# Kernel optimization log

Measured on AMD Instinct MI355X. Metric: run time of the kernel, lower is better.

Reference implementation:

```python
import jax, jax.numpy as jnp
import numpy as np

# pywt Wavelet('db4') decomposition filters (8 taps)
DEC_LO = jnp.array([-0.010597401784997278, 0.032883011666982945, 0.030841381835986965,
                    -0.18703481171888114, -0.02798376941698385, 0.6308807679295904,
                    0.7148465705525415, 0.23037781330885523], dtype=jnp.float32)
DEC_HI = jnp.array([-0.23037781330885523, 0.7148465705525415, -0.6308807679295904,
                    -0.02798376941698385, 0.18703481171888114, 0.030841381835986965,
                    -0.032883011666982945, -0.010597401784997278], dtype=jnp.float32)
FLEN = 8
LEVEL = 3


def _dwt_last(x, f):
    """Single-level DWT along last axis, pywt 'symmetric' mode.
    out[i] = sum_k f[k] * ext[2i+1-k] (true convolution, downsample by 2)."""
    p = FLEN - 1
    pad = [(0, 0)] * (x.ndim - 1) + [(p, p)]
    xp = jnp.pad(x, pad, mode='symmetric')[..., 1:]
    n = x.shape[-1]
    out_len = (n + FLEN - 1) // 2
    f_rev = f[::-1]
    y = f_rev[0] * xp[..., 0:2 * out_len:2]
    for j in range(1, FLEN):  # fixed 8-tap loop
        y = y + f_rev[j] * xp[..., j:j + 2 * out_len:2]
    return y


def _dwt_h(x, f):
    # DWT along axis -2 (rows/H)
    return jnp.swapaxes(_dwt_last(jnp.swapaxes(x, -1, -2), f), -1, -2)


def _dwt2(x):
    # x: [B, H, W] -> (cA, cH, cV, cD), matching pywt dwt2 ('aa','da','ad','dd')
    lo_w = _dwt_last(x, DEC_LO)
    hi_w = _dwt_last(x, DEC_HI)
    cA = _dwt_h(lo_w, DEC_LO)  # low H,  low W
    cH = _dwt_h(lo_w, DEC_HI)  # high H, low W  (horizontal detail)
    cV = _dwt_h(hi_w, DEC_LO)  # low H,  high W (vertical detail)
    cD = _dwt_h(hi_w, DEC_HI)  # high H, high W (diagonal detail)
    return cA, cH, cV, cD


def setup_inputs() -> dict:
    key = jax.random.key(0)
    x = jax.random.normal(key, (16, 1, 1024, 1024), dtype=jnp.float32)
    return {"x": x}


def reference(x):
    # wavedec2 ordering: (cA_L, (cH_L, cV_L, cD_L), ..., (cH_1, cV_1, cD_1))
    a = x[:, 0]  # [B, H, W]
    details = []
    for _ in range(LEVEL):
        a, lh, hl, hh = _dwt2(a)
        details.insert(0, (lh, hl, hh))  # coarsest first, as pywt returns
    outs = [a[:, None]]  # [B,1,h,w]
    for lh, hl, hh in details:
        outs += [lh[:, None], hl[:, None], hh[:, None]]
    return tuple(outs)
```

## Files before the change

### kernel.cpp

```cpp
#include <hip/hip_runtime.h>

typedef float f4 __attribute__((ext_vector_type(4)));
typedef f4 f4u __attribute__((aligned(4)));

__device__ __forceinline__ int refl(int i, int n) {
    i = (i < 0) ? (-i - 1) : i;
    i = (i >= n) ? (2 * n - 1 - i) : i;
    return i;
}

__device__ __forceinline__ unsigned bpack(float lo, float hi) {
    union { float f; unsigned u; } a, b;
    a.f = lo; b.f = hi;
    const unsigned ua = (a.u + 0x7FFFu + ((a.u >> 16) & 1u)) >> 16;
    const unsigned ub = (b.u + 0x7FFFu + ((b.u >> 16) & 1u)) & 0xFFFF0000u;
    return ua | ub;
}
__device__ __forceinline__ float b_lo(unsigned u) {
    union { unsigned u; float f; } x; x.u = u << 16; return x.f;
}
__device__ __forceinline__ float b_hi(unsigned u) {
    union { unsigned u; float f; } x; x.u = u & 0xFFFF0000u; return x.f;
}

__device__ __constant__ const float LOF[8] = {
    -0.010597401784997278f,  0.032883011666982945f,
     0.030841381835986965f, -0.18703481171888114f,
    -0.02798376941698385f,   0.6308807679295904f,
     0.7148465705525415f,    0.23037781330885523f };
__device__ __constant__ const float HIF[8] = {
    -0.23037781330885523f,   0.7148465705525415f,
    -0.6308807679295904f,   -0.02798376941698385f,
     0.18703481171888114f,   0.030841381835986965f,
    -0.032883011666982945f, -0.010597401784997278f };

template<int N, int LDIN, int M, int RPB>
__global__ __launch_bounds__(256, 3)
void dwt_stripe(const float* __restrict__ in, int inb,
                float* __restrict__ oA, int ldA, int Ab,
                float* __restrict__ oH, float* __restrict__ oV,
                float* __restrict__ oD)
{
    constexpr int NG  = (M + 7) / 8;
    constexpr int LDP = 8 * NG;
    constexpr int S   = (M + RPB - 1) / RPB;
    constexpr int HR  = 2 * RPB + 6;
    constexpr int GHI = (N - 16) / 16;
    constexpr int NGI = GHI;
    static_assert(NG - 1 == GHI + 1, "expect exactly 2 edge groups");
    constexpr int NAI = HR * NGI;
    constexpr int NAT = NAI + HR * 2;
    constexpr int NQF = M / 4;
    constexpr int TC  = M - 4 * NQF;
    constexpr int NBM = (RPB / 2) * NQF;
    constexpr int NBT2 = (RPB / 2) * TC;
    constexpr int NB  = NBM + NBT2;

    __shared__ unsigned s[HR * LDP];

    const int G = gridDim.x;
    const int q = G >> 3, rm = G & 7;
    const int xcd = blockIdx.x & 7, pos = blockIdx.x >> 3;
    const int sid = xcd * q + (xcd < rm ? xcd : rm) + pos;
    const int sy = sid % S, b = sid / S;

    const int tid = threadIdx.x;
    const int gr0 = RPB * sy;
    const int rb  = 2 * gr0 - 6;
    const float* Ain = in + b * inb;

    #pragma unroll
    for (int k = 0; k < (NAT + 255) / 256; ++k) {
        const int item = k * 256 + tid;
        if (item < NAI) {
            const int tr = item / NGI;
            const int g  = 1 + (item - tr * NGI);
            const int rr = refl(rb + tr, N);
            const float* p = Ain + rr * LDIN + (16 * g - 8);
            float v[24];
            #pragma unroll
            for (int j = 0; j < 6; ++j) {
                const float4 t4 = *(const float4*)(p + 4 * j);
                v[4*j] = t4.x; v[4*j+1] = t4.y; v[4*j+2] = t4.z; v[4*j+3] = t4.w;
            }
            unsigned w[8];
            #pragma unroll
            for (int d = 0; d < 8; ++d) {
                float lo = 0.f, hi = 0.f;
                #pragma unroll
                for (int t = 0; t < 8; ++t) {
                    const float x = v[2 * d + 9 - t];
                    lo += LOF[t] * x;
                    hi += HIF[t] * x;
                }
                w[d] = bpack(lo, hi);
            }
            unsigned* dst = &s[tr * LDP + 8 * g];
            *(uint4*)(dst)     = make_uint4(w[0], w[1], w[2], w[3]);
            *(uint4*)(dst + 4) = make_uint4(w[4], w[5], w[6], w[7]);
        } else if (item < NAT) {
            const int e  = item - NAI;
            const int tr = e >> 1;
            const int g  = (e & 1) ? (GHI + 1) : 0;
            const int rr = refl(rb + tr, N);
            const float* row = Ain + rr * LDIN;
            const int cb = 16 * g - 8;
            float v[24];
            #pragma unroll
            for (int u = 0; u < 24; ++u) v[u] = row[refl(cb + u, N)];
            unsigned w[8];
            #pragma unroll
            for (int d = 0; d < 8; ++d) {
                float lo = 0.f, hi = 0.f;
                #pragma unroll
                for (int t = 0; t < 8; ++t) {
                    const float x = v[2 * d + 9 - t];
                    lo += LOF[t] * x;
                    hi += HIF[t] * x;
                }
                w[d] = bpack(lo, hi);
            }
            unsigned* dst = &s[tr * LDP + 8 * g];
            *(uint4*)(dst)     = make_uint4(w[0], w[1], w[2], w[3]);
            *(uint4*)(dst + 4) = make_uint4(w[4], w[5], w[6], w[7]);
        }
    }
    __syncthreads();

    #pragma unroll
    for (int k = 0; k < (NB + 255) / 256; ++k) {
        const int item = k * 256 + tid;
        if (item < NBM) {
            const int pr = item / NQF, qc = item - pr * NQF;
            uint4 qv[10];
            #pragma unroll
            for (int j = 0; j < 10; ++j)
                qv[j] = *(const uint4*)&s[(4 * pr + j) * LDP + 4 * qc];

            #pragma unroll
            for (int d = 0; d < 2; ++d) {
                const int gr = gr0 + 2 * pr + d;
                if (gr >= M) continue;
                f4 vA = 0.f, vH = 0.f, vV = 0.f, vD = 0.f;
                #pragma unroll
                for (int t = 0; t < 8; ++t) {
                    const uint4 qq = qv[2 * d + 7 - t];
                    f4 lo, hi;
                    lo.x = b_lo(qq.x); lo.y = b_lo(qq.y); lo.z = b_lo(qq.z); lo.w = b_lo(qq.w);
                    hi.x = b_hi(qq.x); hi.y = b_hi(qq.y); hi.z = b_hi(qq.z); hi.w = b_hi(qq.w);
                    vA += LOF[t] * lo;  vH += HIF[t] * lo;
                    vV += LOF[t] * hi;  vD += HIF[t] * hi;
                }
                const int cq = 4 * qc;
                *(f4u*)&oA[b * Ab + gr * ldA + cq] = vA;
                const int od = b * (M * M) + gr * M + cq;
                *(f4u*)&oH[od] = vH;
                *(f4u*)&oV[od] = vV;
                *(f4u*)&oD[od] = vD;
            }
        } else if (item < NB) {
            const int e = item - NBM;
            const int pr = e % (RPB / 2), c = 4 * NQF + e / (RPB / 2);
            float lov[10], hiv[10];
            #pragma unroll
            for (int j = 0; j < 10; ++j) {
                const unsigned u = s[(4 * pr + j) * LDP + c];
                lov[j] = b_lo(u); hiv[j] = b_hi(u);
            }
            float A0=0.f,H0=0.f,V0=0.f,D0=0.f,A1=0.f,H1=0.f,V1=0.f,D1=0.f;
            #pragma unroll
            for (int t = 0; t < 8; ++t) {
                const float l0 = lov[7 - t], h0 = hiv[7 - t];
                const float l1 = lov[9 - t], h1 = hiv[9 - t];
                A0 += LOF[t] * l0;  H0 += HIF[t] * l0;
                V0 += LOF[t] * h0;  D0 += HIF[t] * h0;
                A1 += LOF[t] * l1;  H1 += HIF[t] * l1;
                V1 += LOF[t] * h1;  D1 += HIF[t] * h1;
            }
            const int gr = gr0 + 2 * pr;
            const int od = b * (M * M) + gr * M + c;
            if (gr < M) {
                oA[b * Ab + gr * ldA + c] = A0;
                oH[od] = H0; oV[od] = V0; oD[od] = D0;
            }
            if (gr + 1 < M) {
                oA[b * Ab + (gr + 1) * ldA + c] = A1;
                oH[od + M] = H1; oV[od + M] = V1; oD[od + M] = D1;
            }
        }
    }
}

#define NTF 512
__global__ __launch_bounds__(NTF, 8)
void dwt2_fused(const float* __restrict__ in, int n, int ldin, int inb,
                int m, int nty, int ntx,
                float* __restrict__ oA, int ldA, int Ab,
                float* __restrict__ oH, float* __restrict__ oV,
                float* __restrict__ oD)
{
    __shared__ unsigned s[70 * 36];

    const int G = gridDim.x;
    const int q = G >> 3, rm = G & 7;
    const int xcd = blockIdx.x & 7, pos = blockIdx.x >> 3;
    const int i = xcd * q + (xcd < rm ? xcd : rm) + pos;
    const int ty = i % nty;
    const int t2 = i / nty;
    const int tx = t2 % ntx;
    const int b  = t2 / ntx;

    const int tid = threadIdx.x;
    const int c0 = tx * 32, r0 = ty * 32;
    const float* Ain = in + b * inb;

    const int rb  = 2 * r0 - 6;
    const int cw0 = 2 * c0 - 8;
    const bool interior = (rb >= 0) && (rb + 69 < n) && (cw0 >= 0) && (cw0 + 71 < n);

    const int tr0 = tid >> 3, g0 = tid & 7;
    const bool has2 = (tid < 48);
    const int tr1 = 64 + (tid >> 3), g1 = tid & 7;

    float v0[16], v1[16];
    if (interior) {
        const float* p0 = Ain + (rb + tr0) * ldin + (cw0 + 8 * g0);
        const float4 a0 = ((const float4*)p0)[0];
        const float4 a1 = ((const float4*)p0)[1];
        const float4 a2 = ((const float4*)p0)[2];
        const float4 a3 = ((const float4*)p0)[3];
        v0[0]=a0.x; v0[1]=a0.y; v0[2]=a0.z; v0[3]=a0.w;
        v0[4]=a1.x; v0[5]=a1.y; v0[6]=a1.z; v0[7]=a1.w;
        v0[8]=a2.x; v0[9]=a2.y; v0[10]=a2.z; v0[11]=a2.w;
        v0[12]=a3.x; v0[13]=a3.y; v0[14]=a3.z; v0[15]=a3.w;
        if (has2) {
            const float* p1 = Ain + (rb + tr1) * ldin + (cw0 + 8 * g1);
            const float4 b0 = ((const float4*)p1)[0];
            const float4 b1 = ((const float4*)p1)[1];
            const float4 b2 = ((const float4*)p1)[2];
            const float4 b3 = ((const float4*)p1)[3];
            v1[0]=b0.x; v1[1]=b0.y; v1[2]=b0.z; v1[3]=b0.w;
            v1[4]=b1.x; v1[5]=b1.y; v1[6]=b1.z; v1[7]=b1.w;
            v1[8]=b2.x; v1[9]=b2.y; v1[10]=b2.z; v1[11]=b2.w;
            v1[12]=b3.x; v1[13]=b3.y; v1[14]=b3.z; v1[15]=b3.w;
        }
    } else {
        const float* row0 = Ain + refl(rb + tr0, n) * ldin;
        const int cb0 = cw0 + 8 * g0;
        #pragma unroll
        for (int u = 0; u < 16; ++u) v0[u] = row0[refl(cb0 + u, n)];
        if (has2) {
            const float* row1 = Ain + refl(rb + tr1, n) * ldin;
            const int cb1 = cw0 + 8 * g1;
            #pragma unroll
            for (int u = 0; u < 16; ++u) v1[u] = row1[refl(cb1 + u, n)];
        }
    }

    {
        unsigned w[4];
        #pragma unroll
        for (int d = 0; d < 4; ++d) {
            float lo = 0.f, hi = 0.f;
            #pragma unroll
            for (int t = 0; t < 8; ++t) {
                const float x = v0[2 * d + 9 - t];
                lo += LOF[t] * x;
                hi += HIF[t] * x;
            }
            w[d] = bpack(lo, hi);
        }
        *(uint4*)&s[tr0 * 36 + 4 * g0] = make_uint4(w[0], w[1], w[2], w[3]);
    }
    if (has2) {
        unsigned w[4];
        #pragma unroll
        for (int d = 0; d < 4; ++d) {
            float lo = 0.f, hi = 0.f;
            #pragma unroll
            for (int t = 0; t < 8; ++t) {
                const float x = v1[2 * d + 9 - t];
                lo += LOF[t] * x;
                hi += HIF[t] * x;
            }
            w[d] = bpack(lo, hi);
        }
        *(uint4*)&s[tr1 * 36 + 4 * g1] = make_uint4(w[0], w[1], w[2], w[3]);
    }
    __syncthreads();

    const int c = tid & 31, pr = tid >> 5;
    float lov[10], hiv[10];
    #pragma unroll
    for (int j = 0; j < 10; ++j) {
        const unsigned u = s[(4 * pr + j) * 36 + c];
        lov[j] = b_lo(u); hiv[j] = b_hi(u);
    }
    float A0=0.f,H0=0.f,V0=0.f,D0=0.f,A1=0.f,H1=0.f,V1=0.f,D1=0.f;
    #pragma unroll
    for (int t = 0; t < 8; ++t) {
        const float l0 = lov[7 - t], h0 = hiv[7 - t];
        const float l1 = lov[9 - t], h1 = hiv[9 - t];
        A0 += LOF[t] * l0;  H0 += HIF[t] * l0;
        V0 += LOF[t] * h0;  D0 += HIF[t] * h0;
        A1 += LOF[t] * l1;  H1 += HIF[t] * l1;
        V1 += LOF[t] * h1;  D1 += HIF[t] * h1;
    }
    const int gr = r0 + 2 * pr, gc = c0 + c;
    if (gc < m) {
        const int ob = b * (m * m);
        const int od = ob + gr * m + gc;
        if (gr < m) {
            oA[b * Ab + gr * ldA + gc] = A0;
            oH[od] = H0; oV[od] = V0; oD[od] = D0;
        }
        if (gr + 1 < m) {
            oA[b * Ab + (gr + 1) * ldA + gc] = A1;
            oH[od + m] = H1; oV[od + m] = V1; oD[od + m] = D1;
        }
    }
}

extern "C" void kernel_launch(void* const* d_in, const int* in_sizes, int n_in,
                              void* d_out, int out_size, void* d_ws, size_t ws_size,
                              hipStream_t stream) {
    const float* x = (const float*)d_in[0];
    float* out = (float*)d_out;
    float* ws  = (float*)d_ws;

    const int B = 16;
    const int m1 = 515, m2 = 261, m3 = 134;
    const int n2 = 515, n3 = 261;

    const int ld1 = 516, b1 = m1 * ld1;
    const int ld2 = 264, b2 = m2 * ld2;
    float* a1 = ws;
    float* a2 = ws + (size_t)b1 * B;

    const size_t sz1 = (size_t)B * m1 * m1;
    const size_t sz2 = (size_t)B * m2 * m2;
    const size_t sz3 = (size_t)B * m3 * m3;

    float* a3  = out;
    float* lh3 = a3  + sz3;
    float* hl3 = lh3 + sz3;
    float* hh3 = hl3 + sz3;
    float* lh2 = hh3 + sz3;
    float* hl2 = lh2 + sz2;
    float* hh2 = hl2 + sz2;
    float* lh1 = hh2 + sz2;
    float* hl1 = lh1 + sz1;
    float* hh1 = hl1 + sz1;

    const int S1 = (m1 + 7) / 8;
    const int t2_ = (m2 + 31) / 32;
    const int t3  = (m3 + 31) / 32;

    dim3 blk(256);
    dwt_stripe<1024, 1024, 515, 8><<<dim3(S1 * B), blk, 0, stream>>>(
        x, 1024 * 1024, a1, ld1, b1, lh1, hl1, hh1);

    dwt2_fused<<<dim3(t2_ * t2_ * B), dim3(NTF), 0, stream>>>(
        a1, n2, ld1, b1, m2, t2_, t2_,
        a2, ld2, b2, lh2, hl2, hh2);

    dwt2_fused<<<dim3(t3 * t3 * B), dim3(NTF), 0, stream>>>(
        a2, n3, ld2, b2, m3, t3, t3,
        a3, m3, m3 * m3, lh3, hl3, hh3);
}
```

Baseline: 52.39 us.

## Widen level-1 stripe to 16 rows with sliding-window vertical pass and swizzled LDS

```diff
diff --git a/kernel.cpp b/kernel.cpp
--- a/kernel.cpp
+++ b/kernel.cpp
@@ -34,27 +34,23 @@
      0.18703481171888114f,   0.030841381835986965f,
     -0.032883011666982945f, -0.010597401784997278f };
 
-template<int N, int LDIN, int M, int RPB>
-__global__ __launch_bounds__(256, 3)
-void dwt_stripe(const float* __restrict__ in, int inb,
-                float* __restrict__ oA, int ldA, int Ab,
-                float* __restrict__ oH, float* __restrict__ oV,
-                float* __restrict__ oD)
+__device__ __forceinline__ int sw(int a) { return a ^ ((a & 96) >> 3); }
+
+#define LDP 520
+#define HR  38
+#define S1N 33
+
+__global__ __launch_bounds__(256, 2)
+void dwt_stripe1(const float* __restrict__ in,
+                 float* __restrict__ oA,
+                 float* __restrict__ oH, float* __restrict__ oV,
+                 float* __restrict__ oD)
 {
-    constexpr int NG  = (M + 7) / 8;
-    constexpr int LDP = 8 * NG;
-    constexpr int S   = (M + RPB - 1) / RPB;
-    constexpr int HR  = 2 * RPB + 6;
-    constexpr int GHI = (N - 16) / 16;
-    constexpr int NGI = GHI;
-    static_assert(NG - 1 == GHI + 1, "expect exactly 2 edge groups");
-    constexpr int NAI = HR * NGI;
-    constexpr int NAT = NAI + HR * 2;
-    constexpr int NQF = M / 4;
-    constexpr int TC  = M - 4 * NQF;
-    constexpr int NBM = (RPB / 2) * NQF;
-    constexpr int NBT2 = (RPB / 2) * TC;
-    constexpr int NB  = NBM + NBT2;
+    constexpr int N = 1024, M = 515;
+    constexpr int ldA = 516, Ab = 516 * 515;
+    constexpr int NAI = HR * 31;
+    constexpr int NAL = NAI + HR;
+    constexpr int NAT = NAL + HR;
 
     __shared__ unsigned s[HR * LDP];
 
@@ -62,30 +58,28 @@
     const int q = G >> 3, rm = G & 7;
     const int xcd = blockIdx.x & 7, pos = blockIdx.x >> 3;
     const int sid = xcd * q + (xcd < rm ? xcd : rm) + pos;
-    const int sy = sid % S, b = sid / S;
+    const int sy = sid % S1N, b = sid / S1N;
 
     const int tid = threadIdx.x;
-    const int gr0 = RPB * sy;
+    const int gr0 = 16 * sy;
     const int rb  = 2 * gr0 - 6;
-    const float* Ain = in + b * inb;
-
-    #pragma unroll
-    for (int k = 0; k < (NAT + 255) / 256; ++k) {
+    const float* Ain = in + b * (N * N);
+
+    for (int k = 0; k < 5; ++k) {
         const int item = k * 256 + tid;
         if (item < NAI) {
-            const int tr = item / NGI;
-            const int g  = 1 + (item - tr * NGI);
+            const int tr = item / 31, g = 1 + (item - (item / 31) * 31);
             const int rr = refl(rb + tr, N);
-            const float* p = Ain + rr * LDIN + (16 * g - 8);
-            float v[24];
-            #pragma unroll
-            for (int j = 0; j < 6; ++j) {
+            const float* p = Ain + rr * N + (32 * g - 8);
+            float v[40];
+            #pragma unroll
+            for (int j = 0; j < 10; ++j) {
                 const float4 t4 = *(const float4*)(p + 4 * j);
                 v[4*j] = t4.x; v[4*j+1] = t4.y; v[4*j+2] = t4.z; v[4*j+3] = t4.w;
             }
-            unsigned w[8];
-            #pragma unroll
-            for (int d = 0; d < 8; ++d) {
+            unsigned w[16];
+            #pragma unroll
+            for (int d = 0; d < 16; ++d) {
                 float lo = 0.f, hi = 0.f;
                 #pragma unroll
                 for (int t = 0; t < 8; ++t) {
@@ -95,97 +89,147 @@
                 }
                 w[d] = bpack(lo, hi);
             }
-            unsigned* dst = &s[tr * LDP + 8 * g];
-            *(uint4*)(dst)     = make_uint4(w[0], w[1], w[2], w[3]);
-            *(uint4*)(dst + 4) = make_uint4(w[4], w[5], w[6], w[7]);
-        } else if (item < NAT) {
-            const int e  = item - NAI;
-            const int tr = e >> 1;
-            const int g  = (e & 1) ? (GHI + 1) : 0;
+            const int dbase = tr * LDP + 16 * g;
+            #pragma unroll
+            for (int j = 0; j < 4; ++j)
+                *(uint4*)&s[sw(dbase + 4 * j)] =
+                    make_uint4(w[4*j], w[4*j+1], w[4*j+2], w[4*j+3]);
+        } else if (item < NAL) {
+            const int tr = item - NAI;
             const int rr = refl(rb + tr, N);
-            const float* row = Ain + rr * LDIN;
-            const int cb = 16 * g - 8;
-            float v[24];
-            #pragma unroll
-            for (int u = 0; u < 24; ++u) v[u] = row[refl(cb + u, N)];
-            unsigned w[8];
-            #pragma unroll
-            for (int d = 0; d < 8; ++d) {
+            const float* p = Ain + rr * N;
+            float v[40];
+            #pragma unroll
+            for (int j = 0; j < 10; ++j) {
+                const float4 t4 = *(const float4*)(p + 4 * j);
+                v[4*j] = t4.x; v[4*j+1] = t4.y; v[4*j+2] = t4.z; v[4*j+3] = t4.w;
+            }
+            unsigned w[16];
+            #pragma unroll
+            for (int d = 0; d < 16; ++d) {
                 float lo = 0.f, hi = 0.f;
                 #pragma unroll
                 for (int t = 0; t < 8; ++t) {
-                    const float x = v[2 * d + 9 - t];
+                    const int ic = 2 * d + 1 - t;
+                    const int vi = (ic < 0) ? (-1 - ic) : ic;
+                    const float x = v[vi];
                     lo += LOF[t] * x;
                     hi += HIF[t] * x;
                 }
                 w[d] = bpack(lo, hi);
             }
-            unsigned* dst = &s[tr * LDP + 8 * g];
-            *(uint4*)(dst)     = make_uint4(w[0], w[1], w[2], w[3]);
-            *(uint4*)(dst + 4) = make_uint4(w[4], w[5], w[6], w[7]);
+            const int dbase = tr * LDP;
+            #pragma unroll
+            for (int j = 0; j < 4; ++j)
+                *(uint4*)&s[sw(dbase + 4 * j)] =
+                    make_uint4(w[4*j], w[4*j+1], w[4*j+2], w[4*j+3]);
+        } else if (item < NAT) {
+            const int tr = item - NAL;
+            const int rr = refl(rb + tr, N);
+            const float* p = Ain + rr * N + 1008;
+            float v[16];
+            #pragma unroll
+            for (int j = 0; j < 4; ++j) {
+                const float4 t4 = *(const float4*)(p + 4 * j);
+                v[4*j] = t4.x; v[4*j+1] = t4.y; v[4*j+2] = t4.z; v[4*j+3] = t4.w;
+            }
+            #pragma unroll
+            for (int d = 0; d < 3; ++d) {
+                float lo = 0.f, hi = 0.f;
+                #pragma unroll
+                for (int t = 0; t < 8; ++t) {
+                    const int ic = 2 * (512 + d) + 1 - t;
+                    const int vi = (ic <= 1023) ? (ic - 1008) : (1039 - ic);
+                    const float x = v[vi];
+                    lo += LOF[t] * x;
+                    hi += HIF[t] * x;
+                }
+                s[sw(tr * LDP + 512 + d)] = bpack(lo, hi);
+            }
         }
     }
     __syncthreads();
 
-    #pragma unroll
-    for (int k = 0; k < (NB + 255) / 256; ++k) {
+    for (int k = 0; k < 2; ++k) {
         const int item = k * 256 + tid;
-        if (item < NBM) {
-            const int pr = item / NQF, qc = item - pr * NQF;
-            uint4 qv[10];
-            #pragma unroll
-            for (int j = 0; j < 10; ++j)
-                qv[j] = *(const uint4*)&s[(4 * pr + j) * LDP + 4 * qc];
-
-            #pragma unroll
-            for (int d = 0; d < 2; ++d) {
-                const int gr = gr0 + 2 * pr + d;
-                if (gr >= M) continue;
-                f4 vA = 0.f, vH = 0.f, vV = 0.f, vD = 0.f;
+        if (item < 256) {
+            const int qc = item & 127, h = item >> 7;
+            const int cq = 4 * qc;
+            const int w0r = 16 * h;
+
+            f4 Lw[10], Hw[10];
+            #pragma unroll
+            for (int j = 0; j < 6; ++j) {
+                const uint4 u = *(const uint4*)&s[sw((w0r + j) * LDP + cq)];
+                Lw[j].x = b_lo(u.x); Lw[j].y = b_lo(u.y); Lw[j].z = b_lo(u.z); Lw[j].w = b_lo(u.w);
+                Hw[j].x = b_hi(u.x); Hw[j].y = b_hi(u.y); Hw[j].z = b_hi(u.z); Hw[j].w = b_hi(u.w);
+            }
+
+            #pragma unroll
+            for (int ph = 0; ph < 4; ++ph) {
+                #pragma unroll
+                for (int j2 = 0; j2 < 4; ++j2) {
+                    const int sl = (6 + 4 * ph + j2) % 10;
+                    const uint4 u = *(const uint4*)&s[sw((w0r + 6 + 4 * ph + j2) * LDP + cq)];
+                    Lw[sl].x = b_lo(u.x); Lw[sl].y = b_lo(u.y); Lw[sl].z = b_lo(u.z); Lw[sl].w = b_lo(u.w);
+                    Hw[sl].x = b_hi(u.x); Hw[sl].y = b_hi(u.y); Hw[sl].z = b_hi(u.z); Hw[sl].w = b_hi(u.w);
+                }
+                f4 A0 = 0.f, H0 = 0.f, V0 = 0.f, D0 = 0.f;
+                f4 A1 = 0.f, H1 = 0.f, V1 = 0.f, D1 = 0.f;
                 #pragma unroll
                 for (int t = 0; t < 8; ++t) {
-                    const uint4 qq = qv[2 * d + 7 - t];
-                    f4 lo, hi;
-                    lo.x = b_lo(qq.x); lo.y = b_lo(qq.y); lo.z = b_lo(qq.z); lo.w = b_lo(qq.w);
-                    hi.x = b_hi(qq.x); hi.y = b_hi(qq.y); hi.z = b_hi(qq.z); hi.w = b_hi(qq.w);
-                    vA += LOF[t] * lo;  vH += HIF[t] * lo;
-                    vV += LOF[t] * hi;  vD += HIF[t] * hi;
-                }
-                const int cq = 4 * qc;
-                *(f4u*)&oA[b * Ab + gr * ldA + cq] = vA;
-                const int od = b * (M * M) + gr * M + cq;
-                *(f4u*)&oH[od] = vH;
-                *(f4u*)&oV[od] = vV;
-                *(f4u*)&oD[od] = vD;
-            }
-        } else if (item < NB) {
-            const int e = item - NBM;
-            const int pr = e % (RPB / 2), c = 4 * NQF + e / (RPB / 2);
-            float lov[10], hiv[10];
-            #pragma unroll
-            for (int j = 0; j < 10; ++j) {
-                const unsigned u = s[(4 * pr + j) * LDP + c];
-                lov[j] = b_lo(u); hiv[j] = b_hi(u);
-            }
-            float A0=0.f,H0=0.f,V0=0.f,D0=0.f,A1=0.f,H1=0.f,V1=0.f,D1=0.f;
-            #pragma unroll
-            for (int t = 0; t < 8; ++t) {
-                const float l0 = lov[7 - t], h0 = hiv[7 - t];
-                const float l1 = lov[9 - t], h1 = hiv[9 - t];
-                A0 += LOF[t] * l0;  H0 += HIF[t] * l0;
-                V0 += LOF[t] * h0;  D0 += HIF[t] * h0;
-                A1 += LOF[t] * l1;  H1 += HIF[t] * l1;
-                V1 += LOF[t] * h1;  D1 += HIF[t] * h1;
-            }
-            const int gr = gr0 + 2 * pr;
-            const int od = b * (M * M) + gr * M + c;
-            if (gr < M) {
-                oA[b * Ab + gr * ldA + c] = A0;
-                oH[od] = H0; oV[od] = V0; oD[od] = D0;
-            }
-            if (gr + 1 < M) {
-                oA[b * Ab + (gr + 1) * ldA + c] = A1;
-                oH[od + M] = H1; oV[od + M] = V1; oD[od + M] = D1;
+                    const f4 l0 = Lw[(4 * ph + 7 - t) % 10], h0 = Hw[(4 * ph + 7 - t) % 10];
+                    const f4 l1 = Lw[(4 * ph + 9 - t) % 10], h1 = Hw[(4 * ph + 9 - t) % 10];
+                    A0 += LOF[t] * l0;  H0 += HIF[t] * l0;
+                    V0 += LOF[t] * h0;  D0 += HIF[t] * h0;
+                    A1 += LOF[t] * l1;  H1 += HIF[t] * l1;
+                    V1 += LOF[t] * h1;  D1 += HIF[t] * h1;
+                }
+                const int gr = gr0 + 8 * h + 2 * ph;
+                if (gr < M) {
+                    *(f4*)&oA[b * Ab + gr * ldA + cq] = A0;
+                    const int od = b * (M * M) + gr * M + cq;
+                    *(f4u*)&oH[od] = H0; *(f4u*)&oV[od] = V0; *(f4u*)&oD[od] = D0;
+                }
+                if (gr + 1 < M) {
+                    *(f4*)&oA[b * Ab + (gr + 1) * ldA + cq] = A1;
+                    const int od = b * (M * M) + (gr + 1) * M + cq;
+                    *(f4u*)&oH[od] = H1; *(f4u*)&oV[od] = V1; *(f4u*)&oD[od] = D1;
+                }
+            }
+        } else if (item < 262) {
+            const int e = item - 256;
+            const int c = 512 + e % 3, h = e / 3;
+            #pragma unroll
+            for (int ph = 0; ph < 4; ++ph) {
+                const int w0 = 16 * h + 4 * ph;
+                float lov[10], hiv[10];
+                #pragma unroll
+                for (int j = 0; j < 10; ++j) {
+                    const unsigned u = s[sw((w0 + j) * LDP + c)];
+                    lov[j] = b_lo(u); hiv[j] = b_hi(u);
+                }
+                float A0=0.f,H0=0.f,V0=0.f,D0=0.f,A1=0.f,H1=0.f,V1=0.f,D1=0.f;
+                #pragma unroll
+                for (int t = 0; t < 8; ++t) {
+                    const float l0 = lov[7 - t], h0 = hiv[7 - t];
+                    const float l1 = lov[9 - t], h1 = hiv[9 - t];
+                    A0 += LOF[t] * l0;  H0 += HIF[t] * l0;
+                    V0 += LOF[t] * h0;  D0 += HIF[t] * h0;
+                    A1 += LOF[t] * l1;  H1 += HIF[t] * l1;
+                    V1 += LOF[t] * h1;  D1 += HIF[t] * h1;
+                }
+                const int gr = gr0 + 8 * h + 2 * ph;
+                if (gr < M) {
+                    oA[b * Ab + gr * ldA + c] = A0;
+                    const int od = b * (M * M) + gr * M + c;
+                    oH[od] = H0; oV[od] = V0; oD[od] = D0;
+                }
+                if (gr + 1 < M) {
+                    oA[b * Ab + (gr + 1) * ldA + c] = A1;
+                    const int od = b * (M * M) + (gr + 1) * M + c;
+                    oH[od] = H1; oV[od] = V1; oD[od] = D1;
+                }
             }
         }
     }
@@ -352,13 +396,11 @@
     float* hl1 = lh1 + sz1;
     float* hh1 = hl1 + sz1;
 
-    const int S1 = (m1 + 7) / 8;
     const int t2_ = (m2 + 31) / 32;
     const int t3  = (m3 + 31) / 32;
 
-    dim3 blk(256);
-    dwt_stripe<1024, 1024, 515, 8><<<dim3(S1 * B), blk, 0, stream>>>(
-        x, 1024 * 1024, a1, ld1, b1, lh1, hl1, hh1);
+    dwt_stripe1<<<dim3(S1N * B), dim3(256), 0, stream>>>(
+        x, a1, lh1, hl1, hh1);
 
     dwt2_fused<<<dim3(t2_ * t2_ * B), dim3(NTF), 0, stream>>>(
         a1, n2, ld1, b1, m2, t2_, t2_,
```

Result: slower. 57.47 us (+9.7%).
